# Kernel optimization log

Measured on AMD Instinct MI355X. Metric: run time of the kernel, lower is better.

## Reference

```python
import jax, jax.numpy as jnp
import numpy as np

B, T, S, H = 8, 512, 512, 768
VOCAB = 32110  # hardcoded in the original module


def setup_inputs() -> dict:
    key = jax.random.key(0)
    k1, k2, k3, k4, k5 = jax.random.split(key, 5)
    return {
        "decoder_input_embeds": jax.random.normal(k1, (B, T, H), dtype=jnp.float32),
        "sequence_output": jax.random.normal(k2, (B, T, H), dtype=jnp.float32),
        "cross_attentions": jax.random.uniform(k3, (B, T, S), dtype=jnp.float32),
        "input_ids_to_copy": jax.random.randint(k4, (B, S), 0, VOCAB, dtype=jnp.int64),
        "w_pgen": jax.random.normal(k5, (2 * H, 1), dtype=jnp.float32) * 0.02,
        "b_pgen": jnp.zeros((1,), dtype=jnp.float32),
    }


def reference(decoder_input_embeds, sequence_output, cross_attentions,
              input_ids_to_copy, w_pgen, b_pgen):
    # p_gen = sigmoid(Linear(concat(dec_embeds, seq_out)))  -> [B, T, 1]
    total_states = jnp.concatenate((decoder_input_embeds, sequence_output), axis=-1)
    p_gen = jax.nn.sigmoid(total_states @ w_pgen + b_pgen)

    # logits[b, t, v] = sum_{s : ids[b,s]==v} attn[b, t, s]
    # (math-equivalent to attn @ one_hot(ids), done as a scatter-add)
    def per_batch(attn_bts, ids_s):  # attn [T, S], ids [S]
        return jax.ops.segment_sum(attn_bts.T, ids_s, num_segments=VOCAB).T  # [T, V]

    logits = jax.vmap(per_batch)(cross_attentions, input_ids_to_copy)  # [B, T, V]
    return p_gen, logits
```

## Files before the change

### kernel.cpp

```cpp
#include <hip/hip_runtime.h>
#include <math.h>

#define BB 8
#define TT 512
#define SS 512
#define HH 768
#define VOCAB 32110
#define HALF0 16056
#define LDSF  16056

__global__ __launch_bounds__(256) void pgen_kernel(
    const float* __restrict__ dec,
    const float* __restrict__ seq,
    const float* __restrict__ w,
    const float* __restrict__ bptr,
    float* __restrict__ out)
{
    const int gid  = blockIdx.x * 256 + threadIdx.x;
    const int row  = gid >> 6;
    const int lane = threadIdx.x & 63;
    if (row >= BB * TT) return;

    const float* d = dec + (size_t)row * HH;
    const float* s = seq + (size_t)row * HH;

    float acc = 0.f;
    #pragma unroll
    for (int j0 = 0; j0 < HH; j0 += 64) {
        int j = j0 + lane;
        acc += d[j] * w[j] + s[j] * w[HH + j];
    }
    #pragma unroll
    for (int off = 32; off > 0; off >>= 1)
        acc += __shfl_down(acc, off, 64);

    if (lane == 0) {
        float x = acc + bptr[0];
        out[row] = 1.f / (1.f + expf(-x));
    }
}

__global__ __launch_bounds__(512, 4) void scatter_logits(
    const float* __restrict__ attn,
    const int*   __restrict__ ids,
    float* __restrict__ out_logits)
{
    __shared__ float smem[LDSF];

    const int bid  = blockIdx.x;
    const int row  = bid >> 1;
    const int half = bid & 1;
    const int lo   = half ? HALF0 : 0;
    const int n    = half ? (VOCAB - HALF0) : HALF0;
    const int b    = row >> 9;
    const int tid  = threadIdx.x;

    float2* sm2 = reinterpret_cast<float2*>(smem);
    #pragma unroll 4
    for (int i = tid; i < LDSF / 2; i += 512) sm2[i] = make_float2(0.f, 0.f);
    __syncthreads();

    {
        const float* arow = attn + (size_t)row * SS;
        const int*   irow = ids  + (size_t)b * SS;
        int   v = irow[tid];
        float a = arow[tid];
        int loc = v - lo;
        if ((unsigned)loc < (unsigned)n) atomicAdd(&smem[loc], a);
    }
    __syncthreads();

    float* dst = out_logits + (size_t)row * VOCAB + lo;
    const float2* src2 = reinterpret_cast<const float2*>(smem);
    float2*       dst2 = reinterpret_cast<float2*>(dst);
    const int n2 = n >> 1;
    for (int i = tid; i < n2; i += 512) dst2[i] = src2[i];
}

extern "C" void kernel_launch(void* const* d_in, const int* in_sizes, int n_in,
                              void* d_out, int out_size, void* d_ws, size_t ws_size,
                              hipStream_t stream) {
    const float* dec  = (const float*)d_in[0];
    const float* seq  = (const float*)d_in[1];
    const float* attn = (const float*)d_in[2];
    const int*   ids  = (const int*)  d_in[3];
    const float* w    = (const float*)d_in[4];
    const float* bp   = (const float*)d_in[5];

    float* out = (float*)d_out;

    pgen_kernel<<<(BB * TT) / 4, 256, 0, stream>>>(dec, seq, w, bp, out);

    scatter_logits<<<BB * TT * 2, 512, 0, stream>>>(attn, ids, out + BB * TT);
}
```

Measured before the change: 544.0 us.

## Split vocab into quarters per row and align logits stores to float4

The scatter kernel now splits each row's vocabulary into four chunks instead of two. This shrinks the shared-memory buffer and allows a higher occupancy bound. Odd rows start only 8-byte aligned in the output, so shared-memory indices are shifted by two floats; this lets the bulk copy use aligned float4 stores, with float2 handling the head and tail. The p_gen dot product is also changed to float4 loads. The cost is four times as many blocks, each of which repeats the id/attention reads and the block-level setup.

```diff
diff --git a/kernel.cpp b/kernel.cpp
--- a/kernel.cpp
+++ b/kernel.cpp
@@ -6,8 +6,9 @@
 #define SS 512
 #define HH 768
 #define VOCAB 32110
-#define HALF0 16056
-#define LDSF  16056
+#define QCHUNK 8028
+#define NROWS (BB * TT)
+#define LDSF (QCHUNK + 4)
 
 __global__ __launch_bounds__(256) void pgen_kernel(
     const float* __restrict__ dec,
@@ -19,16 +20,21 @@
     const int gid  = blockIdx.x * 256 + threadIdx.x;
     const int row  = gid >> 6;
     const int lane = threadIdx.x & 63;
-    if (row >= BB * TT) return;
+    if (row >= NROWS) return;
 
     const float* d = dec + (size_t)row * HH;
     const float* s = seq + (size_t)row * HH;
 
     float acc = 0.f;
     #pragma unroll
-    for (int j0 = 0; j0 < HH; j0 += 64) {
-        int j = j0 + lane;
-        acc += d[j] * w[j] + s[j] * w[HH + j];
+    for (int j0 = 0; j0 < HH; j0 += 256) {
+        int j = j0 + lane * 4;
+        float4 dv = *reinterpret_cast<const float4*>(d + j);
+        float4 wv = *reinterpret_cast<const float4*>(w + j);
+        float4 sv = *reinterpret_cast<const float4*>(s + j);
+        float4 uv = *reinterpret_cast<const float4*>(w + HH + j);
+        acc += dv.x * wv.x + dv.y * wv.y + dv.z * wv.z + dv.w * wv.w;
+        acc += sv.x * uv.x + sv.y * uv.y + sv.z * uv.z + sv.w * uv.w;
     }
     #pragma unroll
     for (int off = 32; off > 0; off >>= 1)
@@ -40,24 +46,26 @@
     }
 }
 
-__global__ __launch_bounds__(512, 4) void scatter_logits(
+__global__ __launch_bounds__(512, 8) void scatter_logits(
     const float* __restrict__ attn,
     const int*   __restrict__ ids,
     float* __restrict__ out_logits)
 {
     __shared__ float smem[LDSF];
 
-    const int bid  = blockIdx.x;
-    const int row  = bid >> 1;
-    const int half = bid & 1;
-    const int lo   = half ? HALF0 : 0;
-    const int n    = half ? (VOCAB - HALF0) : HALF0;
-    const int b    = row >> 9;
-    const int tid  = threadIdx.x;
+    const int bid = blockIdx.x;
+    const int q   = bid >> 12;
+    const int row = bid & (NROWS - 1);
+    const int b   = row >> 9;
+    const int tid = threadIdx.x;
 
-    float2* sm2 = reinterpret_cast<float2*>(smem);
-    #pragma unroll 4
-    for (int i = tid; i < LDSF / 2; i += 512) sm2[i] = make_float2(0.f, 0.f);
+    const int lo    = q * QCHUNK;
+    const int n     = (q == 3) ? (VOCAB - 3 * QCHUNK) : QCHUNK;
+    const int shift = (row & 1) ? 2 : 0;
+
+    float4* sm4 = reinterpret_cast<float4*>(smem);
+    #pragma unroll
+    for (int i = tid; i < LDSF / 4; i += 512) sm4[i] = make_float4(0.f, 0.f, 0.f, 0.f);
     __syncthreads();
 
     {
@@ -66,15 +74,27 @@
         int   v = irow[tid];
         float a = arow[tid];
         int loc = v - lo;
-        if ((unsigned)loc < (unsigned)n) atomicAdd(&smem[loc], a);
+        if ((unsigned)loc < (unsigned)n) atomicAdd(&smem[loc + shift], a);
     }
     __syncthreads();
 
     float* dst = out_logits + (size_t)row * VOCAB + lo;
-    const float2* src2 = reinterpret_cast<const float2*>(smem);
-    float2*       dst2 = reinterpret_cast<float2*>(dst);
-    const int n2 = n >> 1;
-    for (int i = tid; i < n2; i += 512) dst2[i] = src2[i];
+
+    if (shift && tid == 0) {
+        *reinterpret_cast<float2*>(dst) = make_float2(smem[2], smem[3]);
+    }
+    const int main4 = (n - shift) >> 2;
+    const int tail  = n - shift - 4 * main4;
+
+    const float4* s4 = reinterpret_cast<const float4*>(smem + 2 * shift);
+    float4*       d4 = reinterpret_cast<float4*>(dst + shift);
+    #pragma unroll 2
+    for (int i = tid; i < main4; i += 512) d4[i] = s4[i];
+
+    if (tail && tid == 1) {
+        *reinterpret_cast<float2*>(dst + shift + 4 * main4) =
+            *reinterpret_cast<const float2*>(smem + 2 * shift + 4 * main4);
+    }
 }
 
 extern "C" void kernel_launch(void* const* d_in, const int* in_sizes, int n_in,
@@ -89,7 +109,6 @@
 
     float* out = (float*)d_out;
 
-    pgen_kernel<<<(BB * TT) / 4, 256, 0, stream>>>(dec, seq, w, bp, out);
-
-    scatter_logits<<<BB * TT * 2, 512, 0, stream>>>(attn, ids, out + BB * TT);
+    pgen_kernel<<<NROWS / 4, 256, 0, stream>>>(dec, seq, w, bp, out);
+    scatter_logits<<<4 * NROWS, 512, 0, stream>>>(attn, ids, out + NROWS);
 }
```

Result: no change. 550.5 us (+1.2%).
